# Kernel tuning notes

Measured on AMD Instinct MI355X. Metric: run time of the kernel, lower is better.

## Reference

```python
import jax, jax.numpy as jnp
import numpy as np

B, S, H, NH, NKV, HD = 2, 2048, 4096, 32, 8, 128
MAXPOS = 4096

def _rope(x, cos, sin, position_ids):
    # x: [b, h, s, hd]; cos/sin: [maxpos, hd/2]; position_ids: [b, s]
    c = cos[position_ids][:, None]  # [b,1,s,hd/2]
    s_ = sin[position_ids][:, None]
    x1, x2 = x[..., ::2], x[..., 1::2]
    rot = jnp.stack([x1 * c - x2 * s_, x1 * s_ + x2 * c], axis=-1)
    return rot.reshape(x.shape)

def setup_inputs() -> dict:
    key = jax.random.key(0)
    ks = jax.random.split(key, 8)
    hidden_states = jax.random.normal(ks[0], (B, S, H), jnp.float32)
    # realistic RoPE tables
    inv_freq = 1.0 / (10000.0 ** (np.arange(0, HD, 2, dtype=np.float32) / HD))
    t = np.arange(MAXPOS, dtype=np.float32)
    freqs = np.outer(t, inv_freq)  # [maxpos, hd/2]
    cos = jnp.asarray(np.cos(freqs))
    sin = jnp.asarray(np.sin(freqs))
    position_ids = jnp.broadcast_to(jnp.arange(S, dtype=jnp.int64), (B, S))
    # causal additive mask
    neg = jnp.finfo(jnp.float32).min
    causal = jnp.where(jnp.tril(jnp.ones((S, S), bool)), 0.0, neg)
    attention_mask = jnp.broadcast_to(causal, (B, 1, S, S)).astype(jnp.float32)
    sc = 0.02
    Wq = jax.random.normal(ks[1], (NH * HD, H), jnp.float32) * sc
    Wk = jax.random.normal(ks[2], (NKV * HD, H), jnp.float32) * sc
    Wv = jax.random.normal(ks[3], (NKV * HD, H), jnp.float32) * sc
    Wo = jax.random.normal(ks[4], (H, NH * HD), jnp.float32) * sc
    return dict(hidden_states=hidden_states, cos=cos, sin=sin,
                position_ids=position_ids, attention_mask=attention_mask,
                Wq=Wq, Wk=Wk, Wv=Wv, Wo=Wo)

def reference(hidden_states, cos, sin, position_ids, attention_mask, Wq, Wk, Wv, Wo):
    b, s, _ = hidden_states.shape
    groups = NH // NKV
    q = (hidden_states @ Wq.T).reshape(b, s, NH, HD).transpose(0, 2, 1, 3)
    k = (hidden_states @ Wk.T).reshape(b, s, NKV, HD).transpose(0, 2, 1, 3)
    v = (hidden_states @ Wv.T).reshape(b, s, NKV, HD).transpose(0, 2, 1, 3)
    q = _rope(q, cos, sin, position_ids)
    k = _rope(k, cos, sin, position_ids)
    if groups > 1:
        k = jnp.repeat(k, groups, axis=1)
        v = jnp.repeat(v, groups, axis=1)
    scores = jnp.einsum('bhqd,bhkd->bhqk', q, k) / jnp.sqrt(jnp.float32(HD))
    scores = scores + attention_mask
    attn = jax.nn.softmax(scores.astype(jnp.float32), axis=-1).astype(q.dtype)
    out = jnp.einsum('bhqk,bhkd->bhqd', attn, v)
    out = out.transpose(0, 2, 1, 3).reshape(b, s, NH * HD)
    return out @ Wo.T
```

## Files before the change

### kernel.cpp

```cpp
#include <hip/hip_runtime.h>
#include <cstdint>

#define S_   2048
#define H_   4096
#define NH_  32
#define NKV_ 8
#define HD_  128

typedef short  short8  __attribute__((ext_vector_type(8)));
typedef float  floatx4 __attribute__((ext_vector_type(4)));
typedef unsigned int uintx2 __attribute__((ext_vector_type(2)));
typedef unsigned int uint32;
typedef unsigned short ushort16;

__device__ inline unsigned int pk_bf16(float a, float b) {
  unsigned int ua = __builtin_bit_cast(unsigned int, a) + 0x8000u;
  unsigned int ub = __builtin_bit_cast(unsigned int, b) + 0x8000u;
  return __builtin_amdgcn_perm(ub, ua, 0x07060302u);
}
__device__ inline unsigned short f32_bf16(float a) {
  return (unsigned short)((__builtin_bit_cast(unsigned int, a) + 0x8000u) >> 16);
}
__device__ inline float exp2_fast(float x) {
  float r; asm("v_exp_f32 %0, %1" : "=v"(r) : "v"(x)); return r;
}

__device__ inline void gld16(const ushort16* g, ushort16* l) {
  __builtin_amdgcn_global_load_lds((const __attribute__((address_space(1))) void*)g,
                                   (__attribute__((address_space(3))) void*)l, 16, 0, 0);
}

__global__ __launch_bounds__(256)
void cvt_bf16(const float* __restrict__ in, uint32* __restrict__ out) {
  const int idx = blockIdx.x * 256 + threadIdx.x;
  floatx4 v = ((const floatx4*)in)[idx];
  uintx2 o;
  o[0] = pk_bf16(v[0], v[1]);
  o[1] = pk_bf16(v[2], v[3]);
  ((uintx2*)out)[idx] = o;
}

__global__ __launch_bounds__(256)
void transp(const ushort16* __restrict__ in, ushort16* __restrict__ out) {
  __shared__ __align__(16) ushort16 T[64 * 66];
  const int tid = threadIdx.x, wave = tid >> 6, j = tid & 63;
  const int c0 = blockIdx.x * 64, r0 = blockIdx.y * 64;
#pragma unroll
  for (int it = 0; it < 16; it++) {
    const int i = it * 4 + wave;
    T[i * 66 + j] = in[(size_t)(r0 + i) * 1024 + c0 + j];
  }
  __syncthreads();
#pragma unroll
  for (int it = 0; it < 16; it++) {
    const int i = it * 4 + wave;
    out[(size_t)(c0 + i) * 4096 + r0 + j] = T[j * 66 + i];
  }
}

__global__ __launch_bounds__(256)
void gemm128_kv(const ushort16* __restrict__ A, const ushort16* __restrict__ B,
                ushort16* __restrict__ Kout, ushort16* __restrict__ Vout,
                const float* __restrict__ cosT, const float* __restrict__ sinT)
{
  constexpr int K = H_;
  __shared__ __align__(16) ushort16 As[128 * 32];
  __shared__ __align__(16) ushort16 Bs[128 * 32];
  const int bn = blockIdx.x * 128, bm = blockIdx.y * 128;
  const int tid = threadIdx.x, wave = tid >> 6, lane = tid & 63;
  const int l15 = lane & 15, quad = lane >> 4;
  const int wr = (wave & 1) * 64, wc = (wave >> 1) * 64;

  const int crow = lane >> 2;
  const int ckb  = (lane & 3) ^ ((lane >> 3) & 3);
  const int q0 = wave * 2, q1 = q0 + 1;
  const ushort16* gA0 = A + (size_t)(bm + q0 * 16 + crow) * K + ckb * 8;
  const ushort16* gA1 = A + (size_t)(bm + q1 * 16 + crow) * K + ckb * 8;
  const ushort16* gB0 = B + (size_t)(bn + q0 * 16 + crow) * K + ckb * 8;
  const ushort16* gB1 = B + (size_t)(bn + q1 * 16 + crow) * K + ckb * 8;
  ushort16* lA0 = As + q0 * 512;
  ushort16* lA1 = As + q1 * 512;
  ushort16* lB0 = Bs + q0 * 512;
  ushort16* lB1 = Bs + q1 * 512;

  const int slot = quad ^ ((l15 >> 1) & 3);
  int aoff[4], boff[4];
#pragma unroll
  for (int t = 0; t < 4; t++) {
    aoff[t] = (wr + t * 16 + l15) * 32 + slot * 8;
    boff[t] = (wc + t * 16 + l15) * 32 + slot * 8;
  }

  floatx4 acc[4][4] = {};

  for (int k0 = 0; k0 < K; k0 += 32) {
    __syncthreads();
    gld16(gA0 + k0, lA0);
    gld16(gA1 + k0, lA1);
    gld16(gB0 + k0, lB0);
    gld16(gB1 + k0, lB1);
    __syncthreads();

    short8 af[4], bf[4];
#pragma unroll
    for (int t = 0; t < 4; t++) af[t] = *(const short8*)(As + aoff[t]);
#pragma unroll
    for (int t = 0; t < 4; t++) bf[t] = *(const short8*)(Bs + boff[t]);
#pragma unroll
    for (int mt = 0; mt < 4; mt++)
#pragma unroll
      for (int nt = 0; nt < 4; nt++)
        acc[mt][nt] = __builtin_amdgcn_mfma_f32_16x16x32_bf16(af[mt], bf[nt], acc[mt][nt], 0, 0, 0);
  }

#pragma unroll
  for (int mt = 0; mt < 4; mt++) {
#pragma unroll
    for (int nt = 0; nt < 4; nt++) {
      const int col = bn + wc + nt * 16 + l15;
#pragma unroll
      for (int r = 0; r < 4; r++) {
        const int row = bm + wr + mt * 16 + quad * 4 + r;
        float v = acc[mt][nt][r];
        float other = __shfl_xor(v, 1, 64);
        const int pos = row & (S_ - 1);
        const int i   = (col & (HD_ - 1)) >> 1;
        const float c  = cosT[pos * (HD_ / 2) + i];
        const float sn = sinT[pos * (HD_ / 2) + i];
        const float vk = (lane & 1) ? (other * sn + v * c) : (v * c - other * sn);
        if (col < 1024) Kout[(size_t)row * 1024 + col]        = f32_bf16(vk);
        else            Vout[(size_t)row * 1024 + col - 1024] = f32_bf16(v);
      }
    }
  }
}

template<bool ROPE, bool SCALE, bool OUTF32>
__global__ __launch_bounds__(512, 2)
void gemm256(const ushort16* __restrict__ A, const ushort16* __restrict__ B,
             void* __restrict__ Y, int N,
             const float* __restrict__ cosT, const float* __restrict__ sinT)
{
  constexpr int NT = H_ / 64;
  __shared__ __align__(16) ushort16 LA[2][16384];
  __shared__ __align__(16) ushort16 LB[2][16384];

  const int bid = (int)blockIdx.x;
  const int wg  = (bid & 7) * ((int)gridDim.x >> 3) + (bid >> 3);
  const int nbx = N >> 8;
  const int bm = (wg / nbx) * 256, bn = (wg % nbx) * 256;

  const int tid = threadIdx.x, wave = tid >> 6, lane = tid & 63;
  const int l15 = lane & 15, quad = lane >> 4;
  const int wm = wave >> 2, wn = wave & 3;

  const int s1 = 512 + tid;
  const int off0 = (tid >> 3) * 4096 + (((tid & 7) ^ ((tid >> 3) & 7)) * 8);
  const int off1 = (s1  >> 3) * 4096 + (((s1  & 7) ^ ((s1  >> 3) & 7)) * 8);

  auto STG_A = [&](int kt, int h) {
    const ushort16* g = A + (size_t)(bm + h * 128) * 4096 + kt * 64;
    ushort16* d = &LA[kt & 1][h * 8192 + wave * 512];
    gld16(g + off0, d);
    gld16(g + off1, d + 4096);
  };
  auto STG_B = [&](int kt, int h) {
    const ushort16* g = B + (size_t)(bn + h * 128) * 4096 + kt * 64;
    ushort16* d = &LB[kt & 1][h * 8192 + wave * 512];
    gld16(g + off0, d);
    gld16(g + off1, d + 4096);
  };

  const int slotk0 = ((0 * 4 + quad) ^ (l15 & 7)) * 8;
  const int slotk1 = ((1 * 4 + quad) ^ (l15 & 7)) * 8;

  short8 fragA[4][2];
  short8 b10[2], b11[2];
  short8 b0a0[2], b0a1[2];
  short8 b0b0[2], b0b1[2];
  floatx4 acc[8][4] = {};

#define G256_LDA(CA_, jm0)                                                    \
  do {                                                                        \
    _Pragma("unroll") for (int j = 0; j < 4; j++) {                           \
      const int R = (2 * ((jm0) + j) + wm) * 16 + l15;                        \
      fragA[j][0] = *(const short8*)((CA_) + R * 64 + slotk0);                \
      fragA[j][1] = *(const short8*)((CA_) + R * 64 + slotk1);                \
    }                                                                         \
  } while (0)

#define G256_LDB(LB_, jn0, D0, D1)                                            \
  do {                                                                        \
    { const int R = (4 * (jn0) + wn) * 16 + l15;                              \
      D0[0] = *(const short8*)((LB_) + R * 64 + slotk0);                      \
      D0[1] = *(const short8*)((LB_) + R * 64 + slotk1); }                    \
    { const int R = (4 * ((jn0) + 1) + wn) * 16 + l15;                        \
      D1[0] = *(const short8*)((LB_) + R * 64 + slotk0);                      \
      D1[1] = *(const short8*)((LB_) + R * 64 + slotk1); }                    \
  } while (0)

#define G256_MM(jm0, jn0, B0, B1)                                             \
  do {                                                                        \
    __builtin_amdgcn_s_setprio(1);                                            \
    _Pragma("unroll") for (int j = 0; j < 4; j++) {                           \
      acc[(jm0) + j][(jn0)] =                                                 \
          __builtin_amdgcn_mfma_f32_16x16x32_bf16(fragA[j][0], B0[0], acc[(jm0) + j][(jn0)], 0, 0, 0); \
      acc[(jm0) + j][(jn0)] =                                                 \
          __builtin_amdgcn_mfma_f32_16x16x32_bf16(fragA[j][1], B0[1], acc[(jm0) + j][(jn0)], 0, 0, 0); \
      acc[(jm0) + j][(jn0) + 1] =                                             \
          __builtin_amdgcn_mfma_f32_16x16x32_bf16(fragA[j][0], B1[0], acc[(jm0) + j][(jn0) + 1], 0, 0, 0); \
      acc[(jm0) + j][(jn0) + 1] =                                             \
          __builtin_amdgcn_mfma_f32_16x16x32_bf16(fragA[j][1], B1[1], acc[(jm0) + j][(jn0) + 1], 0, 0, 0); \
    }                                                                         \
    __builtin_amdgcn_s_setprio(0);                                            \
  } while (0)

#define BARRIER __builtin_amdgcn_s_barrier()
#define LGK0 do { asm volatile("s_waitcnt lgkmcnt(0)" ::: "memory");          \
                  __builtin_amdgcn_sched_barrier(0); } while (0)
#define VMC(t) do {                                                           \
    if ((t) < NT - 2) asm volatile("s_waitcnt vmcnt(6)" ::: "memory");        \
    else              asm volatile("s_waitcnt vmcnt(0)" ::: "memory");        \
  } while (0)

#define G256_TILE(t, C0, C1, N0, N1)                                          \
  do {                                                                        \
    const ushort16* CA_ = &LA[(t) & 1][0];                                    \
    const ushort16* CB_ = &LB[(t) & 1][0];                                    \
                                                    \
    G256_LDA(CA_, 0);                                                         \
    if ((t) + 1 < NT) STG_A((t) + 1, 0);                                      \
    BARRIER; LGK0;                                                            \
    G256_MM(0, 0, C0, C1);                                                    \
    VMC(t); BARRIER;                                                          \
                                                    \
    G256_LDB(CB_, 2, b10, b11);                                               \
    if ((t) + 1 < NT) STG_B((t) + 1, 1);                                      \
    BARRIER; LGK0;                                                            \
    G256_MM(0, 2, b10, b11);                                                  \
    VMC(t); BARRIER;                                                          \
                                                    \
    G256_LDA(CA_, 4);                                                         \
    if ((t) + 1 < NT) STG_A((t) + 1, 1);                                      \
    BARRIER; LGK0;                                                            \
    G256_MM(4, 2, b10, b11);                                                  \
    VMC(t); BARRIER;                                                          \
      \
    if ((t) + 1 < NT) G256_LDB(&LB[((t) + 1) & 1][0], 0, N0, N1);             \
    if ((t) + 2 < NT) STG_B((t) + 2, 0);                                      \
    BARRIER;                                                                  \
    G256_MM(4, 0, C0, C1);                                                    \
    VMC(t); BARRIER;                                                          \
  } while (0)

  STG_B(0, 0);
  STG_A(0, 0);
  asm volatile("s_waitcnt vmcnt(0)" ::: "memory");
  BARRIER;
  G256_LDB(&LB[0][0], 0, b0a0, b0a1);
  STG_B(0, 1);
  STG_A(0, 1);
  STG_B(1, 0);

#pragma unroll 1
  for (int t0 = 0; t0 < NT; t0 += 2) {
    G256_TILE(t0,     b0a0, b0a1, b0b0, b0b1);
    G256_TILE(t0 + 1, b0b0, b0b1, b0a0, b0a1);
  }

#undef G256_LDA
#undef G256_LDB
#undef G256_MM
#undef G256_TILE
#undef BARRIER
#undef LGK0
#undef VMC

#pragma unroll
  for (int jm = 0; jm < 8; jm++) {
#pragma unroll
    for (int jn = 0; jn < 4; jn++) {
      const int col = bn + (4 * jn + wn) * 16 + l15;
#pragma unroll
      for (int r = 0; r < 4; r++) {
        const int row = bm + (2 * jm + wm) * 16 + quad * 4 + r;
        float v = acc[jm][jn][r];
        if (ROPE) {
          float other = __shfl_xor(v, 1, 64);
          const int pos = row & (S_ - 1);
          const int i   = (col & (HD_ - 1)) >> 1;
          const float c  = cosT[pos * (HD_ / 2) + i];
          const float sn = sinT[pos * (HD_ / 2) + i];
          v = (lane & 1) ? (other * sn + v * c) : (v * c - other * sn);
        }
        if (SCALE) v *= (0.08838834764831845f * 1.4426950408889634f);
        if (OUTF32) ((float*)Y)[(size_t)row * N + col] = v;
        else        ((ushort16*)Y)[(size_t)row * N + col] = f32_bf16(v);
      }
    }
  }
}

__global__ __launch_bounds__(512, 4)
void flash_mfma(const ushort16* __restrict__ Qg, const ushort16* __restrict__ Kg,
                const ushort16* __restrict__ Vtg, ushort16* __restrict__ Cg)
{
  __shared__ __align__(16) ushort16 Ks[2][64 * 128];
  __shared__ __align__(16) ushort16 VT[2][128 * 64];
  __shared__ __align__(16) ushort16 Ps[8][16 * 64];

  const int tid = threadIdx.x, wave = tid >> 6, lane = tid & 63;
  const int l15 = lane & 15, quad = lane >> 4;
  const int qb = 15 - (int)blockIdx.x;
  const int by = blockIdx.y;
  const int b = by >> 5, h = by & 31, kh = h >> 2;
  const int qrow0 = qb * 128 + wave * 16;

  short8 aq[4];
  const ushort16* qbase = Qg + (size_t)(b * S_ + qrow0 + l15) * 4096 + h * 128 + quad * 8;
#pragma unroll
  for (int ks = 0; ks < 4; ks++) aq[ks] = *(const short8*)(qbase + ks * 32);

  int kOff[2], vOff[2];
#pragma unroll
  for (int it = 0; it < 2; it++) {
    const int s = it * 512 + tid;
    const int rK = s >> 4, cK = (s & 15) ^ (rK & 15);
    kOff[it] = rK * 1024 + cK * 8;
    const int dV = s >> 3, cV = (s & 7) ^ (dV & 7);
    vOff[it] = dV * 4096 + cV * 8;
  }
  const ushort16* Kbase = Kg + (size_t)(b * S_) * 1024 + kh * 128;
  const ushort16* Vbase = Vtg + (size_t)(kh * 128) * 4096 + (size_t)b * S_;
  const int ktmax = 2 * qb + 1;

  auto STAGE = [&](int kt, int buf) {
    const ushort16* kg = Kbase + (size_t)kt * 65536;
    const ushort16* vg = Vbase + kt * 64;
#pragma unroll
    for (int it = 0; it < 2; it++) {
      gld16(kg + kOff[it], &Ks[buf][0] + it * 4096 + wave * 512);
      gld16(vg + vOff[it], &VT[buf][0] + it * 4096 + wave * 512);
    }
  };

  STAGE(0, 0);
  __syncthreads();

  floatx4 o_acc[8] = {};
  float m_i = -1e30f, l_i = 0.f;
  ushort16* Pw = &Ps[wave][0];

  for (int kt = 0; kt <= ktmax; ++kt) {
    const int cur = kt & 1;
    if (kt < ktmax) STAGE(kt + 1, cur ^ 1);
    const ushort16* KsC = &Ks[cur][0];
    const ushort16* VTC = &VT[cur][0];

    if (kt * 64 <= qrow0 + 15) {
      floatx4 st[4] = {};
      __builtin_amdgcn_s_setprio(1);
#pragma unroll
      for (int k4 = 0; k4 < 4; k4++)
#pragma unroll
        for (int ks = 0; ks < 4; ks++) {
          short8 ak = *(const short8*)(KsC + (k4 * 16 + l15) * 128 + (((ks * 4 + quad) ^ l15) * 8));
          st[k4] = __builtin_amdgcn_mfma_f32_16x16x32_bf16(ak, aq[ks], st[k4], 0, 0, 0);
        }
      __builtin_amdgcn_s_setprio(0);

      if (kt * 64 + 63 > qrow0) {
        const int q = qrow0 + l15;
#pragma unroll
        for (int k4 = 0; k4 < 4; k4++) {
          const int key = kt * 64 + k4 * 16 + quad * 4;
#pragma unroll
          for (int r = 0; r < 4; r++)
            if (key + r > q) st[k4][r] = -1e30f;
        }
      }

      float mx = st[0][0];
#pragma unroll
      for (int k4 = 0; k4 < 4; k4++)
#pragma unroll
        for (int r = 0; r < 4; r++) mx = fmaxf(mx, st[k4][r]);
      mx = fmaxf(mx, __shfl_xor(mx, 16, 64));
      mx = fmaxf(mx, __shfl_xor(mx, 32, 64));

      if (!__all(mx - m_i <= 8.f)) {
        const float mn = fmaxf(m_i, mx);
        const float alpha = exp2_fast(m_i - mn);
        m_i = mn;
        l_i *= alpha;
        float ar[4];
#pragma unroll
        for (int r = 0; r < 4; r++) ar[r] = __shfl(alpha, quad * 4 + r, 64);
#pragma unroll
        for (int dt = 0; dt < 8; dt++)
#pragma unroll
          for (int r = 0; r < 4; r++) o_acc[dt][r] *= ar[r];
      }
      const float m = m_i;

      float rs = 0.f;
#pragma unroll
      for (int k4 = 0; k4 < 4; k4++) {
        const float p0 = exp2_fast(st[k4][0] - m);
        const float p1 = exp2_fast(st[k4][1] - m);
        const float p2 = exp2_fast(st[k4][2] - m);
        const float p3 = exp2_fast(st[k4][3] - m);
        rs += (p0 + p1) + (p2 + p3);
        uintx2 w;
        w[0] = pk_bf16(p0, p1);
        w[1] = pk_bf16(p2, p3);
        *(uintx2*)(Pw + l15 * 64 + (((k4 * 2 + (quad >> 1)) ^ (l15 & 7)) * 8) + (quad & 1) * 4) = w;
      }
      rs += __shfl_xor(rs, 16, 64);
      rs += __shfl_xor(rs, 32, 64);
      l_i += rs;

      __builtin_amdgcn_s_setprio(1);
#pragma unroll
      for (int ks2 = 0; ks2 < 2; ks2++) {
        short8 ap = *(const short8*)(Pw + l15 * 64 + (((ks2 * 4 + quad) ^ (l15 & 7)) * 8));
#pragma unroll
        for (int dt = 0; dt < 8; dt++) {
          short8 bv = *(const short8*)(VTC + (dt * 16 + l15) * 64 + (((ks2 * 4 + quad) ^ (l15 & 7)) * 8));
          o_acc[dt] = __builtin_amdgcn_mfma_f32_16x16x32_bf16(ap, bv, o_acc[dt], 0, 0, 0);
        }
      }
      __builtin_amdgcn_s_setprio(0);
    }
    __syncthreads();
  }

  const float linv = 1.f / l_i;
  float vr[4];
#pragma unroll
  for (int r = 0; r < 4; r++) vr[r] = __shfl(linv, quad * 4 + r, 64);
#pragma unroll
  for (int dt = 0; dt < 8; dt++)
#pragma unroll
    for (int r = 0; r < 4; r++)
      Cg[(size_t)(b * S_ + qrow0 + quad * 4 + r) * 4096 + h * 128 + dt * 16 + l15] =
          f32_bf16(o_acc[dt][r] * vr[r]);
}

extern "C" void kernel_launch(void* const* d_in, const int* in_sizes, int n_in,
                              void* d_out, int out_size, void* d_ws, size_t ws_size,
                              hipStream_t stream) {
  const float* hs   = (const float*)d_in[0];
  const float* cosT = (const float*)d_in[1];
  const float* sinT = (const float*)d_in[2];
  const float* Wq = (const float*)d_in[5];
  const float* Wk = (const float*)d_in[6];
  const float* Wv = (const float*)d_in[7];
  const float* Wo = (const float*)d_in[8];
  float* out = (float*)d_out;

  char* ws = (char*)d_ws;
  ushort16* hsB = (ushort16*)(ws);
  ushort16* QB  = (ushort16*)(ws + 33554432);
  ushort16* KB  = (ushort16*)(ws + 67108864);
  ushort16* VB  = (ushort16*)(ws + 75497472);
  ushort16* VTg = (ushort16*)(ws + 83886080);
  ushort16* WB  = (ushort16*)(ws + 92274688);
  ushort16* CB  = hsB;

  dim3 blk(256);
  cvt_bf16<<<dim3(16384), blk, 0, stream>>>(hs, (uint32*)hsB);
  cvt_bf16<<<dim3(16384), blk, 0, stream>>>(Wq, (uint32*)WB);
  gemm256<true,  true,  false><<<dim3(256), dim3(512), 0, stream>>>(hsB, WB, QB, 4096, cosT, sinT);
  cvt_bf16<<<dim3(4096),  blk, 0, stream>>>(Wk, (uint32*)WB);
  cvt_bf16<<<dim3(4096),  blk, 0, stream>>>(Wv, (uint32*)(WB + 4194304));
  gemm128_kv<<<dim3(16, 32), blk, 0, stream>>>(hsB, WB, KB, VB, cosT, sinT);
  transp<<<dim3(16, 64), blk, 0, stream>>>(VB, VTg);
  flash_mfma<<<dim3(16, 2 * NH_), dim3(512), 0, stream>>>(QB, KB, VTg, CB);
  cvt_bf16<<<dim3(16384), blk, 0, stream>>>(Wo, (uint32*)WB);
  gemm256<false, false, true><<<dim3(256), dim3(512), 0, stream>>>(CB, WB, out, 4096, cosT, sinT);
}
```

Measured before the change: 744.6 us.

## Double flash-attention query tile per wave to reuse K/V loads across two row blocks

Each wave now processes 32 query rows as two 16-row MFMA tiles, so each block covers 256 queries and every K and V fragment read from LDS feeds two MFMAs. This halves K/V staging traffic per query and amortizes barriers. The grid is reordered so heads vary along x and query blocks (largest first) along y. The cost is more registers (launch bounds drop to 2 blocks per CU), a larger P scratch buffer, and coarser causal load balancing with fewer, longer blocks.

```diff
diff --git a/kernel.cpp b/kernel.cpp
--- a/kernel.cpp
+++ b/kernel.cpp
@@ -227,25 +227,21 @@
   do {                                                                        \
     const ushort16* CA_ = &LA[(t) & 1][0];                                    \
     const ushort16* CB_ = &LB[(t) & 1][0];                                    \
-                                                    \
     G256_LDA(CA_, 0);                                                         \
     if ((t) + 1 < NT) STG_A((t) + 1, 0);                                      \
     BARRIER; LGK0;                                                            \
     G256_MM(0, 0, C0, C1);                                                    \
     VMC(t); BARRIER;                                                          \
-                                                    \
     G256_LDB(CB_, 2, b10, b11);                                               \
     if ((t) + 1 < NT) STG_B((t) + 1, 1);                                      \
     BARRIER; LGK0;                                                            \
     G256_MM(0, 2, b10, b11);                                                  \
     VMC(t); BARRIER;                                                          \
-                                                    \
     G256_LDA(CA_, 4);                                                         \
     if ((t) + 1 < NT) STG_A((t) + 1, 1);                                      \
     BARRIER; LGK0;                                                            \
     G256_MM(4, 2, b10, b11);                                                  \
     VMC(t); BARRIER;                                                          \
-      \
     if ((t) + 1 < NT) G256_LDB(&LB[((t) + 1) & 1][0], 0, N0, N1);             \
     if ((t) + 2 < NT) STG_B((t) + 2, 0);                                      \
     BARRIER;                                                                  \
@@ -301,25 +297,28 @@
   }
 }
 
-__global__ __launch_bounds__(512, 4)
+__global__ __launch_bounds__(512, 2)
 void flash_mfma(const ushort16* __restrict__ Qg, const ushort16* __restrict__ Kg,
                 const ushort16* __restrict__ Vtg, ushort16* __restrict__ Cg)
 {
   __shared__ __align__(16) ushort16 Ks[2][64 * 128];
   __shared__ __align__(16) ushort16 VT[2][128 * 64];
-  __shared__ __align__(16) ushort16 Ps[8][16 * 64];
+  __shared__ __align__(16) ushort16 Ps[8][32 * 64];
 
   const int tid = threadIdx.x, wave = tid >> 6, lane = tid & 63;
   const int l15 = lane & 15, quad = lane >> 4;
-  const int qb = 15 - (int)blockIdx.x;
-  const int by = blockIdx.y;
-  const int b = by >> 5, h = by & 31, kh = h >> 2;
-  const int qrow0 = qb * 128 + wave * 16;
-
-  short8 aq[4];
+  const int bh = (int)blockIdx.x;
+  const int qb = 7 - (int)blockIdx.y;
+  const int b = bh >> 5, h = bh & 31, kh = h >> 2;
+  const int qrow0 = qb * 256 + wave * 32;
+
+  short8 aq[2][4];
   const ushort16* qbase = Qg + (size_t)(b * S_ + qrow0 + l15) * 4096 + h * 128 + quad * 8;
 #pragma unroll
-  for (int ks = 0; ks < 4; ks++) aq[ks] = *(const short8*)(qbase + ks * 32);
+  for (int mt = 0; mt < 2; mt++)
+#pragma unroll
+    for (int ks = 0; ks < 4; ks++)
+      aq[mt][ks] = *(const short8*)(qbase + mt * 16 * 4096 + ks * 32);
 
   int kOff[2], vOff[2];
 #pragma unroll
@@ -332,7 +331,7 @@
   }
   const ushort16* Kbase = Kg + (size_t)(b * S_) * 1024 + kh * 128;
   const ushort16* Vbase = Vtg + (size_t)(kh * 128) * 4096 + (size_t)b * S_;
-  const int ktmax = 2 * qb + 1;
+  const int ktmax = 4 * qb + 3;
 
   auto STAGE = [&](int kt, int buf) {
     const ushort16* kg = Kbase + (size_t)kt * 65536;
@@ -347,8 +346,8 @@
   STAGE(0, 0);
   __syncthreads();
 
-  floatx4 o_acc[8] = {};
-  float m_i = -1e30f, l_i = 0.f;
+  floatx4 o0[8] = {}, o1[8] = {};
+  float m0 = -1e30f, m1 = -1e30f, l0 = 0.f, l1 = 0.f;
   ushort16* Pw = &Ps[wave][0];
 
   for (int kt = 0; kt <= ktmax; ++kt) {
@@ -357,77 +356,86 @@
     const ushort16* KsC = &Ks[cur][0];
     const ushort16* VTC = &VT[cur][0];
 
-    if (kt * 64 <= qrow0 + 15) {
-      floatx4 st[4] = {};
+    if (kt * 64 <= qrow0 + 31) {
+      floatx4 s0[4] = {}, s1[4] = {};
       __builtin_amdgcn_s_setprio(1);
 #pragma unroll
       for (int k4 = 0; k4 < 4; k4++)
 #pragma unroll
         for (int ks = 0; ks < 4; ks++) {
           short8 ak = *(const short8*)(KsC + (k4 * 16 + l15) * 128 + (((ks * 4 + quad) ^ l15) * 8));
-          st[k4] = __builtin_amdgcn_mfma_f32_16x16x32_bf16(ak, aq[ks], st[k4], 0, 0, 0);
+          s0[k4] = __builtin_amdgcn_mfma_f32_16x16x32_bf16(ak, aq[0][ks], s0[k4], 0, 0, 0);
+          s1[k4] = __builtin_amdgcn_mfma_f32_16x16x32_bf16(ak, aq[1][ks], s1[k4], 0, 0, 0);
         }
       __builtin_amdgcn_s_setprio(0);
 
       if (kt * 64 + 63 > qrow0) {
-        const int q = qrow0 + l15;
 #pragma unroll
         for (int k4 = 0; k4 < 4; k4++) {
           const int key = kt * 64 + k4 * 16 + quad * 4;
 #pragma unroll
-          for (int r = 0; r < 4; r++)
-            if (key + r > q) st[k4][r] = -1e30f;
+          for (int r = 0; r < 4; r++) {
+            if (key + r > qrow0 + l15)      s0[k4][r] = -1e30f;
+            if (key + r > qrow0 + 16 + l15) s1[k4][r] = -1e30f;
+          }
         }
       }
 
-      float mx = st[0][0];
-#pragma unroll
-      for (int k4 = 0; k4 < 4; k4++)
-#pragma unroll
-        for (int r = 0; r < 4; r++) mx = fmaxf(mx, st[k4][r]);
-      mx = fmaxf(mx, __shfl_xor(mx, 16, 64));
-      mx = fmaxf(mx, __shfl_xor(mx, 32, 64));
-
-      if (!__all(mx - m_i <= 8.f)) {
-        const float mn = fmaxf(m_i, mx);
-        const float alpha = exp2_fast(m_i - mn);
-        m_i = mn;
-        l_i *= alpha;
-        float ar[4];
-#pragma unroll
-        for (int r = 0; r < 4; r++) ar[r] = __shfl(alpha, quad * 4 + r, 64);
-#pragma unroll
-        for (int dt = 0; dt < 8; dt++)
-#pragma unroll
-          for (int r = 0; r < 4; r++) o_acc[dt][r] *= ar[r];
+#define FL_SOFTMAX(sv, m_i, l_i, ov, PBASE)                                   \
+      {                                                                       \
+        float mx = sv[0][0];                                                  \
+        _Pragma("unroll") for (int k4 = 0; k4 < 4; k4++)                      \
+          _Pragma("unroll") for (int r = 0; r < 4; r++)                       \
+            mx = fmaxf(mx, sv[k4][r]);                                        \
+        mx = fmaxf(mx, __shfl_xor(mx, 16, 64));                               \
+        mx = fmaxf(mx, __shfl_xor(mx, 32, 64));                               \
+        if (!__all(mx - m_i <= 8.f)) {                                        \
+          const float mn = fmaxf(m_i, mx);                                    \
+          const float alpha = exp2_fast(m_i - mn);                            \
+          m_i = mn;                                                           \
+          l_i *= alpha;                                                       \
+          float ar[4];                                                        \
+          _Pragma("unroll") for (int r = 0; r < 4; r++)                       \
+            ar[r] = __shfl(alpha, quad * 4 + r, 64);                          \
+          _Pragma("unroll") for (int dt = 0; dt < 8; dt++)                    \
+            _Pragma("unroll") for (int r = 0; r < 4; r++)                     \
+              ov[dt][r] *= ar[r];                                             \
+        }                                                                     \
+        const float m = m_i;                                                  \
+        float rs = 0.f;                                                       \
+        _Pragma("unroll") for (int k4 = 0; k4 < 4; k4++) {                    \
+          const float p0 = exp2_fast(sv[k4][0] - m);                          \
+          const float p1 = exp2_fast(sv[k4][1] - m);                          \
+          const float p2 = exp2_fast(sv[k4][2] - m);                          \
+          const float p3 = exp2_fast(sv[k4][3] - m);                          \
+          rs += (p0 + p1) + (p2 + p3);                                        \
+          uintx2 w;                                                           \
+          w[0] = pk_bf16(p0, p1);                                             \
+          w[1] = pk_bf16(p2, p3);                                             \
+          *(uintx2*)(Pw + (PBASE) + l15 * 64 +                                \
+                     (((k4 * 2 + (quad >> 1)) ^ (l15 & 7)) * 8) +             \
+                     (quad & 1) * 4) = w;                                     \
+        }                                                                     \
+        rs += __shfl_xor(rs, 16, 64);                                         \
+        rs += __shfl_xor(rs, 32, 64);                                         \
+        l_i += rs;                                                            \
       }
-      const float m = m_i;
-
-      float rs = 0.f;
-#pragma unroll
-      for (int k4 = 0; k4 < 4; k4++) {
-        const float p0 = exp2_fast(st[k4][0] - m);
-        const float p1 = exp2_fast(st[k4][1] - m);
-        const float p2 = exp2_fast(st[k4][2] - m);
-        const float p3 = exp2_fast(st[k4][3] - m);
-        rs += (p0 + p1) + (p2 + p3);
-        uintx2 w;
-        w[0] = pk_bf16(p0, p1);
-        w[1] = pk_bf16(p2, p3);
-        *(uintx2*)(Pw + l15 * 64 + (((k4 * 2 + (quad >> 1)) ^ (l15 & 7)) * 8) + (quad & 1) * 4) = w;
-      }
-      rs += __shfl_xor(rs, 16, 64);
-      rs += __shfl_xor(rs, 32, 64);
-      l_i += rs;
+
+      FL_SOFTMAX(s0, m0, l0, o0, 0)
+      FL_SOFTMAX(s1, m1, l1, o1, 1024)
+#undef FL_SOFTMAX
 
       __builtin_amdgcn_s_setprio(1);
 #pragma unroll
       for (int ks2 = 0; ks2 < 2; ks2++) {
-        short8 ap = *(const short8*)(Pw + l15 * 64 + (((ks2 * 4 + quad) ^ (l15 & 7)) * 8));
+        const int pswz = (((ks2 * 4 + quad) ^ (l15 & 7)) * 8);
+        short8 ap0 = *(const short8*)(Pw + l15 * 64 + pswz);
+        short8 ap1 = *(const short8*)(Pw + 1024 + l15 * 64 + pswz);
 #pragma unroll
         for (int dt = 0; dt < 8; dt++) {
-          short8 bv = *(const short8*)(VTC + (dt * 16 + l15) * 64 + (((ks2 * 4 + quad) ^ (l15 & 7)) * 8));
-          o_acc[dt] = __builtin_amdgcn_mfma_f32_16x16x32_bf16(ap, bv, o_acc[dt], 0, 0, 0);
+          short8 bv = *(const short8*)(VTC + (dt * 16 + l15) * 64 + pswz);
+          o0[dt] = __builtin_amdgcn_mfma_f32_16x16x32_bf16(ap0, bv, o0[dt], 0, 0, 0);
+          o1[dt] = __builtin_amdgcn_mfma_f32_16x16x32_bf16(ap1, bv, o1[dt], 0, 0, 0);
         }
       }
       __builtin_amdgcn_s_setprio(0);
@@ -435,16 +443,30 @@
     __syncthreads();
   }
 
-  const float linv = 1.f / l_i;
-  float vr[4];
-#pragma unroll
-  for (int r = 0; r < 4; r++) vr[r] = __shfl(linv, quad * 4 + r, 64);
-#pragma unroll
-  for (int dt = 0; dt < 8; dt++)
-#pragma unroll
-    for (int r = 0; r < 4; r++)
-      Cg[(size_t)(b * S_ + qrow0 + quad * 4 + r) * 4096 + h * 128 + dt * 16 + l15] =
-          f32_bf16(o_acc[dt][r] * vr[r]);
+  {
+    const float li0 = 1.f / l0;
+    float vr[4];
+#pragma unroll
+    for (int r = 0; r < 4; r++) vr[r] = __shfl(li0, quad * 4 + r, 64);
+#pragma unroll
+    for (int dt = 0; dt < 8; dt++)
+#pragma unroll
+      for (int r = 0; r < 4; r++)
+        Cg[(size_t)(b * S_ + qrow0 + quad * 4 + r) * 4096 + h * 128 + dt * 16 + l15] =
+            f32_bf16(o0[dt][r] * vr[r]);
+  }
+  {
+    const float li1 = 1.f / l1;
+    float vr[4];
+#pragma unroll
+    for (int r = 0; r < 4; r++) vr[r] = __shfl(li1, quad * 4 + r, 64);
+#pragma unroll
+    for (int dt = 0; dt < 8; dt++)
+#pragma unroll
+      for (int r = 0; r < 4; r++)
+        Cg[(size_t)(b * S_ + qrow0 + 16 + quad * 4 + r) * 4096 + h * 128 + dt * 16 + l15] =
+            f32_bf16(o1[dt][r] * vr[r]);
+  }
 }
 
 extern "C" void kernel_launch(void* const* d_in, const int* in_sizes, int n_in,
@@ -476,7 +498,7 @@
   cvt_bf16<<<dim3(4096),  blk, 0, stream>>>(Wv, (uint32*)(WB + 4194304));
   gemm128_kv<<<dim3(16, 32), blk, 0, stream>>>(hsB, WB, KB, VB, cosT, sinT);
   transp<<<dim3(16, 64), blk, 0, stream>>>(VB, VTg);
-  flash_mfma<<<dim3(16, 2 * NH_), dim3(512), 0, stream>>>(QB, KB, VTg, CB);
+  flash_mfma<<<dim3(64, 8), dim3(512), 0, stream>>>(QB, KB, VTg, CB);
   cvt_bf16<<<dim3(16384), blk, 0, stream>>>(Wo, (uint32*)WB);
   gemm256<false, false, true><<<dim3(256), dim3(512), 0, stream>>>(CB, WB, out, 4096, cosT, sinT);
 }
```

Result: faster. 703.5 us (-5.5%).
